# Optimization experiments

Measured on AMD Instinct MI355X. Metric: run time of the kernel, lower is better.

## Reference

```python
import jax, jax.numpy as jnp
import numpy as np

N_NODES = 2_000_000
N_GRAPHS = 8192
C = 128


def setup_inputs() -> dict:
    key = jax.random.key(0)
    k1, k2, k3, k4 = jax.random.split(key, 4)
    x = jax.random.normal(k1, (N_NODES, C), dtype=jnp.float32)
    batch = jnp.sort(jax.random.randint(k2, (N_NODES,), 0, N_GRAPHS, dtype=jnp.int64))
    # nn.Linear(2C -> C): stored here as (2C, C) so out = merged @ W + b
    W = jax.random.normal(k3, (2 * C, C), dtype=jnp.float32) * (1.0 / np.sqrt(2 * C))
    b = jax.random.normal(k4, (C,), dtype=jnp.float32) * 0.01
    return {"x": x, "batch": batch, "W": W, "b": b}


def reference(x, batch, W, b):
    # segment mean: sum / count (guard empty segments)
    seg_sum = jax.ops.segment_sum(x, batch, num_segments=N_GRAPHS)          # [G, C]
    counts = jax.ops.segment_sum(jnp.ones((x.shape[0],), x.dtype), batch,
                                 num_segments=N_GRAPHS)                      # [G]
    safe_counts = jnp.maximum(counts, 1.0)[:, None]
    mean_pooled = seg_sum / safe_counts                                      # [G, C]
    # segment max (replace -inf from empty segments with 0)
    seg_max = jax.ops.segment_max(x, batch, num_segments=N_GRAPHS)          # [G, C]
    max_pooled = jnp.where(counts[:, None] > 0, seg_max, 0.0)
    merged = jnp.concatenate([mean_pooled, max_pooled], axis=1)              # [G, 2C]
    alpha = jax.nn.sigmoid(merged @ W + b)                                   # [G, C]
    return alpha * mean_pooled + (1.0 - alpha) * max_pooled
```

## Files before the change

kernel.cpp:

```cpp
#include <hip/hip_runtime.h>
#include <math.h>

#define N_NODES  2000000
#define N_GRAPHS 8192
#define CDIM     128
#define G_PER    16
#define RED_BLOCKS 2048

__device__ __forceinline__ void atomicMaxF(float* addr, float v) {
    if (v >= 0.0f) {
        atomicMax((int*)addr, __float_as_int(v));
    } else {
        atomicMin((unsigned int*)addr, __float_as_uint(v));
    }
}

__global__ __launch_bounds__(256) void init_kernel(float4* __restrict__ seg_sum4,
                                                   float4* __restrict__ seg_max4) {
    int i = blockIdx.x * blockDim.x + threadIdx.x;
    const int total4 = N_GRAPHS * CDIM / 4;
    if (i < total4) {
        float ninf = -__builtin_huge_valf();
        seg_sum4[i] = make_float4(0.f, 0.f, 0.f, 0.f);
        seg_max4[i] = make_float4(ninf, ninf, ninf, ninf);
    }
}

__global__ __launch_bounds__(256) void count_kernel(const int* __restrict__ batch,
                                                    int* __restrict__ counts) {
    int g = blockIdx.x * blockDim.x + threadIdx.x;
    if (g >= N_GRAPHS) return;
    int lo = 0, hi = N_NODES;
    while (lo < hi) { int mid = (lo + hi) >> 1; if (batch[mid] < g) lo = mid + 1; else hi = mid; }
    int start = lo;
    hi = N_NODES;
    while (lo < hi) { int mid = (lo + hi) >> 1; if (batch[mid] < g + 1) lo = mid + 1; else hi = mid; }
    counts[g] = lo - start;
}

__global__ __launch_bounds__(256) void reduce_kernel(const float4* __restrict__ x4,
                                                     const int* __restrict__ batch,
                                                     float* __restrict__ seg_sum,
                                                     float* __restrict__ seg_max,
                                                     int rows_per_block) {
    const int start = blockIdx.x * rows_per_block;
    const int end   = min(start + rows_per_block, N_NODES);
    const int q  = threadIdx.x & 31;
    const int rl = threadIdx.x >> 5;

    const float ninf = -__builtin_huge_valf();
    float4 s = make_float4(0.f, 0.f, 0.f, 0.f);
    float4 m = make_float4(ninf, ninf, ninf, ninf);
    int cur = -1;

    for (int r = start + rl; r < end; r += 8) {
        int seg = batch[r];
        float4 v = x4[(size_t)r * (CDIM / 4) + q];
        if (seg != cur) {
            if (cur >= 0) {
                float* sp = seg_sum + (size_t)cur * CDIM + q * 4;
                float* mp = seg_max + (size_t)cur * CDIM + q * 4;
                atomicAdd(sp + 0, s.x); atomicAdd(sp + 1, s.y);
                atomicAdd(sp + 2, s.z); atomicAdd(sp + 3, s.w);
                atomicMaxF(mp + 0, m.x); atomicMaxF(mp + 1, m.y);
                atomicMaxF(mp + 2, m.z); atomicMaxF(mp + 3, m.w);
            }
            cur = seg;
            s = make_float4(0.f, 0.f, 0.f, 0.f);
            m = make_float4(ninf, ninf, ninf, ninf);
        }
        s.x += v.x; s.y += v.y; s.z += v.z; s.w += v.w;
        m.x = fmaxf(m.x, v.x); m.y = fmaxf(m.y, v.y);
        m.z = fmaxf(m.z, v.z); m.w = fmaxf(m.w, v.w);
    }
    if (cur >= 0) {
        float* sp = seg_sum + (size_t)cur * CDIM + q * 4;
        float* mp = seg_max + (size_t)cur * CDIM + q * 4;
        atomicAdd(sp + 0, s.x); atomicAdd(sp + 1, s.y);
        atomicAdd(sp + 2, s.z); atomicAdd(sp + 3, s.w);
        atomicMaxF(mp + 0, m.x); atomicMaxF(mp + 1, m.y);
        atomicMaxF(mp + 2, m.z); atomicMaxF(mp + 3, m.w);
    }
}

__global__ __launch_bounds__(256) void final_kernel(const float* __restrict__ seg_sum,
                                                    const float* __restrict__ seg_max,
                                                    const int* __restrict__ counts,
                                                    const float* __restrict__ W,
                                                    const float* __restrict__ bias,
                                                    float* __restrict__ out) {
    __shared__ float mean_s[G_PER][CDIM];
    __shared__ float maxx_s[G_PER][CDIM];

    const int g0  = blockIdx.x * G_PER;
    const int tid = threadIdx.x;

    for (int idx = tid; idx < G_PER * CDIM; idx += 256) {
        int gl = idx >> 7;
        int ch = idx & (CDIM - 1);
        int g  = g0 + gl;
        int cnt = counts[g];
        float mv = 0.f, xv = 0.f;
        if (cnt > 0) {
            float inv = 1.0f / (float)cnt;
            mv = seg_sum[(size_t)g * CDIM + ch] * inv;
            xv = seg_max[(size_t)g * CDIM + ch];
        }
        mean_s[gl][ch] = mv;
        maxx_s[gl][ch] = xv;
    }
    __syncthreads();

    const int j0    = (tid & 63) * 2;
    const int gbase = (tid >> 6) * 4;

    float acc[4][2];
#pragma unroll
    for (int gl = 0; gl < 4; gl++) { acc[gl][0] = 0.f; acc[gl][1] = 0.f; }

#pragma unroll 4
    for (int kq = 0; kq < CDIM / 4; kq++) {
        int k = kq * 4;
        float2 w0 = *(const float2*)(W + (size_t)(k + 0) * CDIM + j0);
        float2 w1 = *(const float2*)(W + (size_t)(k + 1) * CDIM + j0);
        float2 w2 = *(const float2*)(W + (size_t)(k + 2) * CDIM + j0);
        float2 w3 = *(const float2*)(W + (size_t)(k + 3) * CDIM + j0);
#pragma unroll
        for (int gl = 0; gl < 4; gl++) {
            float4 mv = *(const float4*)&mean_s[gbase + gl][k];
            acc[gl][0] += mv.x * w0.x + mv.y * w1.x + mv.z * w2.x + mv.w * w3.x;
            acc[gl][1] += mv.x * w0.y + mv.y * w1.y + mv.z * w2.y + mv.w * w3.y;
        }
    }
#pragma unroll 4
    for (int kq = 0; kq < CDIM / 4; kq++) {
        int k = kq * 4;
        const float* Wr = W + (size_t)(CDIM + k) * CDIM + j0;
        float2 w0 = *(const float2*)(Wr + 0 * CDIM);
        float2 w1 = *(const float2*)(Wr + 1 * CDIM);
        float2 w2 = *(const float2*)(Wr + 2 * CDIM);
        float2 w3 = *(const float2*)(Wr + 3 * CDIM);
#pragma unroll
        for (int gl = 0; gl < 4; gl++) {
            float4 xv = *(const float4*)&maxx_s[gbase + gl][k];
            acc[gl][0] += xv.x * w0.x + xv.y * w1.x + xv.z * w2.x + xv.w * w3.x;
            acc[gl][1] += xv.x * w0.y + xv.y * w1.y + xv.z * w2.y + xv.w * w3.y;
        }
    }

    float2 bb = *(const float2*)(bias + j0);
#pragma unroll
    for (int gl = 0; gl < 4; gl++) {
        int g = g0 + gbase + gl;
        float z0 = acc[gl][0] + bb.x;
        float z1 = acc[gl][1] + bb.y;
        float a0 = 1.0f / (1.0f + expf(-z0));
        float a1 = 1.0f / (1.0f + expf(-z1));
        float m0 = mean_s[gbase + gl][j0 + 0];
        float m1 = mean_s[gbase + gl][j0 + 1];
        float x0 = maxx_s[gbase + gl][j0 + 0];
        float x1 = maxx_s[gbase + gl][j0 + 1];
        float2 o;
        o.x = a0 * m0 + (1.0f - a0) * x0;
        o.y = a1 * m1 + (1.0f - a1) * x1;
        *(float2*)(out + (size_t)g * CDIM + j0) = o;
    }
}

extern "C" void kernel_launch(void* const* d_in, const int* in_sizes, int n_in,
                              void* d_out, int out_size, void* d_ws, size_t ws_size,
                              hipStream_t stream) {
    const float* x     = (const float*)d_in[0];
    const int*   batch = (const int*)d_in[1];
    const float* W     = (const float*)d_in[2];
    const float* bias  = (const float*)d_in[3];
    float*       out   = (float*)d_out;

    float* seg_sum = (float*)d_ws;
    float* seg_max = seg_sum + (size_t)N_GRAPHS * CDIM;
    int*   counts  = (int*)(seg_max + (size_t)N_GRAPHS * CDIM);

    {
        int total4 = N_GRAPHS * CDIM / 4;
        int blocks = (total4 + 255) / 256;
        init_kernel<<<blocks, 256, 0, stream>>>((float4*)seg_sum, (float4*)seg_max);
    }
    count_kernel<<<N_GRAPHS / 256, 256, 0, stream>>>(batch, counts);
    {
        int rpb = (N_NODES + RED_BLOCKS - 1) / RED_BLOCKS;
        reduce_kernel<<<RED_BLOCKS, 256, 0, stream>>>((const float4*)x, batch,
                                                      seg_sum, seg_max, rpb);
    }
    final_kernel<<<N_GRAPHS / G_PER, 256, 0, stream>>>(seg_sum, seg_max, counts,
                                                       W, bias, out);
}
```

Baseline: 1.532 ms.

## Fuse segment reduction with gating via per-graph segment offsets, drop atomics

```diff
diff --git a/kernel.cpp b/kernel.cpp
--- a/kernel.cpp
+++ b/kernel.cpp
@@ -4,167 +4,138 @@
 #define N_NODES  2000000
 #define N_GRAPHS 8192
 #define CDIM     128
-#define G_PER    16
-#define RED_BLOCKS 2048
+#define GPB      4
 
-__device__ __forceinline__ void atomicMaxF(float* addr, float v) {
-    if (v >= 0.0f) {
-        atomicMax((int*)addr, __float_as_int(v));
+__global__ __launch_bounds__(256) void starts_kernel(const int* __restrict__ batch,
+                                                     int* __restrict__ starts) {
+    int i = blockIdx.x * blockDim.x + threadIdx.x;
+    if (i >= N_NODES) return;
+    int b = batch[i];
+    if (i == 0) {
+        for (int g = 0; g <= b; ++g) starts[g] = 0;
+    }
+    if (i == N_NODES - 1) {
+        for (int g = b + 1; g <= N_GRAPHS; ++g) starts[g] = N_NODES;
     } else {
-        atomicMin((unsigned int*)addr, __float_as_uint(v));
+        int bn = batch[i + 1];
+        for (int g = b + 1; g <= bn; ++g) starts[g] = i + 1;
     }
 }
 
-__global__ __launch_bounds__(256) void init_kernel(float4* __restrict__ seg_sum4,
-                                                   float4* __restrict__ seg_max4) {
-    int i = blockIdx.x * blockDim.x + threadIdx.x;
-    const int total4 = N_GRAPHS * CDIM / 4;
-    if (i < total4) {
-        float ninf = -__builtin_huge_valf();
-        seg_sum4[i] = make_float4(0.f, 0.f, 0.f, 0.f);
-        seg_max4[i] = make_float4(ninf, ninf, ninf, ninf);
-    }
-}
-
-__global__ __launch_bounds__(256) void count_kernel(const int* __restrict__ batch,
-                                                    int* __restrict__ counts) {
-    int g = blockIdx.x * blockDim.x + threadIdx.x;
-    if (g >= N_GRAPHS) return;
-    int lo = 0, hi = N_NODES;
-    while (lo < hi) { int mid = (lo + hi) >> 1; if (batch[mid] < g) lo = mid + 1; else hi = mid; }
-    int start = lo;
-    hi = N_NODES;
-    while (lo < hi) { int mid = (lo + hi) >> 1; if (batch[mid] < g + 1) lo = mid + 1; else hi = mid; }
-    counts[g] = lo - start;
-}
-
-__global__ __launch_bounds__(256) void reduce_kernel(const float4* __restrict__ x4,
-                                                     const int* __restrict__ batch,
-                                                     float* __restrict__ seg_sum,
-                                                     float* __restrict__ seg_max,
-                                                     int rows_per_block) {
-    const int start = blockIdx.x * rows_per_block;
-    const int end   = min(start + rows_per_block, N_NODES);
-    const int q  = threadIdx.x & 31;
-    const int rl = threadIdx.x >> 5;
-
-    const float ninf = -__builtin_huge_valf();
-    float4 s = make_float4(0.f, 0.f, 0.f, 0.f);
-    float4 m = make_float4(ninf, ninf, ninf, ninf);
-    int cur = -1;
-
-    for (int r = start + rl; r < end; r += 8) {
-        int seg = batch[r];
-        float4 v = x4[(size_t)r * (CDIM / 4) + q];
-        if (seg != cur) {
-            if (cur >= 0) {
-                float* sp = seg_sum + (size_t)cur * CDIM + q * 4;
-                float* mp = seg_max + (size_t)cur * CDIM + q * 4;
-                atomicAdd(sp + 0, s.x); atomicAdd(sp + 1, s.y);
-                atomicAdd(sp + 2, s.z); atomicAdd(sp + 3, s.w);
-                atomicMaxF(mp + 0, m.x); atomicMaxF(mp + 1, m.y);
-                atomicMaxF(mp + 2, m.z); atomicMaxF(mp + 3, m.w);
-            }
-            cur = seg;
-            s = make_float4(0.f, 0.f, 0.f, 0.f);
-            m = make_float4(ninf, ninf, ninf, ninf);
-        }
-        s.x += v.x; s.y += v.y; s.z += v.z; s.w += v.w;
-        m.x = fmaxf(m.x, v.x); m.y = fmaxf(m.y, v.y);
-        m.z = fmaxf(m.z, v.z); m.w = fmaxf(m.w, v.w);
-    }
-    if (cur >= 0) {
-        float* sp = seg_sum + (size_t)cur * CDIM + q * 4;
-        float* mp = seg_max + (size_t)cur * CDIM + q * 4;
-        atomicAdd(sp + 0, s.x); atomicAdd(sp + 1, s.y);
-        atomicAdd(sp + 2, s.z); atomicAdd(sp + 3, s.w);
-        atomicMaxF(mp + 0, m.x); atomicMaxF(mp + 1, m.y);
-        atomicMaxF(mp + 2, m.z); atomicMaxF(mp + 3, m.w);
-    }
-}
-
-__global__ __launch_bounds__(256) void final_kernel(const float* __restrict__ seg_sum,
-                                                    const float* __restrict__ seg_max,
-                                                    const int* __restrict__ counts,
+__global__ __launch_bounds__(256) void fused_kernel(const float4* __restrict__ x4,
+                                                    const int* __restrict__ starts,
                                                     const float* __restrict__ W,
                                                     const float* __restrict__ bias,
                                                     float* __restrict__ out) {
-    __shared__ float mean_s[G_PER][CDIM];
-    __shared__ float maxx_s[G_PER][CDIM];
+    __shared__ float mean_s[GPB][CDIM];
+    __shared__ float maxx_s[GPB][CDIM];
+    __shared__ float red_sum[4][CDIM];
+    __shared__ float red_max[4][CDIM];
 
-    const int g0  = blockIdx.x * G_PER;
-    const int tid = threadIdx.x;
+    const int tid  = threadIdx.x;
+    const int q    = tid & 31;
+    const int rl   = tid >> 5;
+    const int wave = tid >> 6;
+    const int lane = tid & 63;
+    const int g0   = blockIdx.x * GPB;
+    const float ninf = -__builtin_huge_valf();
 
-    for (int idx = tid; idx < G_PER * CDIM; idx += 256) {
-        int gl = idx >> 7;
-        int ch = idx & (CDIM - 1);
-        int g  = g0 + gl;
-        int cnt = counts[g];
-        float mv = 0.f, xv = 0.f;
-        if (cnt > 0) {
-            float inv = 1.0f / (float)cnt;
-            mv = seg_sum[(size_t)g * CDIM + ch] * inv;
-            xv = seg_max[(size_t)g * CDIM + ch];
+    for (int gl = 0; gl < GPB; ++gl) {
+        const int s0 = starts[g0 + gl];
+        const int s1 = starts[g0 + gl + 1];
+
+        float4 s = make_float4(0.f, 0.f, 0.f, 0.f);
+        float4 m = make_float4(ninf, ninf, ninf, ninf);
+
+        int r = s0 + rl;
+        for (; r + 8 < s1; r += 16) {
+            float4 v0 = x4[(size_t)r       * (CDIM / 4) + q];
+            float4 v1 = x4[(size_t)(r + 8) * (CDIM / 4) + q];
+            s.x += v0.x + v1.x; s.y += v0.y + v1.y;
+            s.z += v0.z + v1.z; s.w += v0.w + v1.w;
+            m.x = fmaxf(m.x, fmaxf(v0.x, v1.x));
+            m.y = fmaxf(m.y, fmaxf(v0.y, v1.y));
+            m.z = fmaxf(m.z, fmaxf(v0.z, v1.z));
+            m.w = fmaxf(m.w, fmaxf(v0.w, v1.w));
         }
-        mean_s[gl][ch] = mv;
-        maxx_s[gl][ch] = xv;
+        if (r < s1) {
+            float4 v = x4[(size_t)r * (CDIM / 4) + q];
+            s.x += v.x; s.y += v.y; s.z += v.z; s.w += v.w;
+            m.x = fmaxf(m.x, v.x); m.y = fmaxf(m.y, v.y);
+            m.z = fmaxf(m.z, v.z); m.w = fmaxf(m.w, v.w);
+        }
+
+        s.x += __shfl_xor(s.x, 32); s.y += __shfl_xor(s.y, 32);
+        s.z += __shfl_xor(s.z, 32); s.w += __shfl_xor(s.w, 32);
+        m.x = fmaxf(m.x, __shfl_xor(m.x, 32));
+        m.y = fmaxf(m.y, __shfl_xor(m.y, 32));
+        m.z = fmaxf(m.z, __shfl_xor(m.z, 32));
+        m.w = fmaxf(m.w, __shfl_xor(m.w, 32));
+
+        if (lane < 32) {
+            *(float4*)&red_sum[wave][q * 4] = s;
+            *(float4*)&red_max[wave][q * 4] = m;
+        }
+        __syncthreads();
+
+        if (tid < CDIM) {
+            float ssum = red_sum[0][tid] + red_sum[1][tid]
+                       + red_sum[2][tid] + red_sum[3][tid];
+            float smax = fmaxf(fmaxf(red_max[0][tid], red_max[1][tid]),
+                               fmaxf(red_max[2][tid], red_max[3][tid]));
+            int cnt = s1 - s0;
+            float mv = 0.f, xv = 0.f;
+            if (cnt > 0) {
+                mv = ssum / (float)cnt;
+                xv = smax;
+            }
+            mean_s[gl][tid] = mv;
+            maxx_s[gl][tid] = xv;
+        }
+        __syncthreads();
     }
-    __syncthreads();
 
-    const int j0    = (tid & 63) * 2;
-    const int gbase = (tid >> 6) * 4;
-
-    float acc[4][2];
-#pragma unroll
-    for (int gl = 0; gl < 4; gl++) { acc[gl][0] = 0.f; acc[gl][1] = 0.f; }
+    const int j0 = (tid & 63) * 2;
+    const int gw = wave;
+    float acc0 = 0.f, acc1 = 0.f;
 
 #pragma unroll 4
-    for (int kq = 0; kq < CDIM / 4; kq++) {
+    for (int kq = 0; kq < CDIM / 4; ++kq) {
         int k = kq * 4;
         float2 w0 = *(const float2*)(W + (size_t)(k + 0) * CDIM + j0);
         float2 w1 = *(const float2*)(W + (size_t)(k + 1) * CDIM + j0);
         float2 w2 = *(const float2*)(W + (size_t)(k + 2) * CDIM + j0);
         float2 w3 = *(const float2*)(W + (size_t)(k + 3) * CDIM + j0);
-#pragma unroll
-        for (int gl = 0; gl < 4; gl++) {
-            float4 mv = *(const float4*)&mean_s[gbase + gl][k];
-            acc[gl][0] += mv.x * w0.x + mv.y * w1.x + mv.z * w2.x + mv.w * w3.x;
-            acc[gl][1] += mv.x * w0.y + mv.y * w1.y + mv.z * w2.y + mv.w * w3.y;
-        }
+        float4 mv = *(const float4*)&mean_s[gw][k];
+        acc0 += mv.x * w0.x + mv.y * w1.x + mv.z * w2.x + mv.w * w3.x;
+        acc1 += mv.x * w0.y + mv.y * w1.y + mv.z * w2.y + mv.w * w3.y;
     }
 #pragma unroll 4
-    for (int kq = 0; kq < CDIM / 4; kq++) {
+    for (int kq = 0; kq < CDIM / 4; ++kq) {
         int k = kq * 4;
         const float* Wr = W + (size_t)(CDIM + k) * CDIM + j0;
         float2 w0 = *(const float2*)(Wr + 0 * CDIM);
         float2 w1 = *(const float2*)(Wr + 1 * CDIM);
         float2 w2 = *(const float2*)(Wr + 2 * CDIM);
         float2 w3 = *(const float2*)(Wr + 3 * CDIM);
-#pragma unroll
-        for (int gl = 0; gl < 4; gl++) {
-            float4 xv = *(const float4*)&maxx_s[gbase + gl][k];
-            acc[gl][0] += xv.x * w0.x + xv.y * w1.x + xv.z * w2.x + xv.w * w3.x;
-            acc[gl][1] += xv.x * w0.y + xv.y * w1.y + xv.z * w2.y + xv.w * w3.y;
-        }
+        float4 xv = *(const float4*)&maxx_s[gw][k];
+        acc0 += xv.x * w0.x + xv.y * w1.x + xv.z * w2.x + xv.w * w3.x;
+        acc1 += xv.x * w0.y + xv.y * w1.y + xv.z * w2.y + xv.w * w3.y;
     }
 
     float2 bb = *(const float2*)(bias + j0);
-#pragma unroll
-    for (int gl = 0; gl < 4; gl++) {
-        int g = g0 + gbase + gl;
-        float z0 = acc[gl][0] + bb.x;
-        float z1 = acc[gl][1] + bb.y;
-        float a0 = 1.0f / (1.0f + expf(-z0));
-        float a1 = 1.0f / (1.0f + expf(-z1));
-        float m0 = mean_s[gbase + gl][j0 + 0];
-        float m1 = mean_s[gbase + gl][j0 + 1];
-        float x0 = maxx_s[gbase + gl][j0 + 0];
-        float x1 = maxx_s[gbase + gl][j0 + 1];
-        float2 o;
-        o.x = a0 * m0 + (1.0f - a0) * x0;
-        o.y = a1 * m1 + (1.0f - a1) * x1;
-        *(float2*)(out + (size_t)g * CDIM + j0) = o;
-    }
+    float z0 = acc0 + bb.x;
+    float z1 = acc1 + bb.y;
+    float a0 = 1.0f / (1.0f + expf(-z0));
+    float a1 = 1.0f / (1.0f + expf(-z1));
+    float m0 = mean_s[gw][j0 + 0];
+    float m1 = mean_s[gw][j0 + 1];
+    float x0 = maxx_s[gw][j0 + 0];
+    float x1 = maxx_s[gw][j0 + 1];
+    float2 o;
+    o.x = a0 * m0 + (1.0f - a0) * x0;
+    o.y = a1 * m1 + (1.0f - a1) * x1;
+    *(float2*)(out + (size_t)(g0 + gw) * CDIM + j0) = o;
 }
 
 extern "C" void kernel_launch(void* const* d_in, const int* in_sizes, int n_in,
@@ -176,21 +147,10 @@
     const float* bias  = (const float*)d_in[3];
     float*       out   = (float*)d_out;
 
-    float* seg_sum = (float*)d_ws;
-    float* seg_max = seg_sum + (size_t)N_GRAPHS * CDIM;
-    int*   counts  = (int*)(seg_max + (size_t)N_GRAPHS * CDIM);
+    int* starts = (int*)d_ws;
 
-    {
-        int total4 = N_GRAPHS * CDIM / 4;
-        int blocks = (total4 + 255) / 256;
-        init_kernel<<<blocks, 256, 0, stream>>>((float4*)seg_sum, (float4*)seg_max);
-    }
-    count_kernel<<<N_GRAPHS / 256, 256, 0, stream>>>(batch, counts);
-    {
-        int rpb = (N_NODES + RED_BLOCKS - 1) / RED_BLOCKS;
-        reduce_kernel<<<RED_BLOCKS, 256, 0, stream>>>((const float4*)x, batch,
-                                                      seg_sum, seg_max, rpb);
-    }
-    final_kernel<<<N_GRAPHS / G_PER, 256, 0, stream>>>(seg_sum, seg_max, counts,
-                                                       W, bias, out);
+    starts_kernel<<<(N_NODES + 255) / 256, 256, 0, stream>>>(batch, starts);
+
+    fused_kernel<<<N_GRAPHS / GPB, 256, 0, stream>>>((const float4*)x, starts,
+                                                     W, bias, out);
 }
```

After: 1.334 ms. 12.9% less time.
